# Performance work log

Hardware: AMD Instinct MI355X
Metric: run time of the kernel (lower is better)

Reference implementation:

```python
import jax, jax.numpy as jnp
import numpy as np

N = 50000      # nodes
E = 400000     # edges (avg degree 8)
N_IN = 256     # n_in_chan
N_HID = 256    # n_hid_chan


def gcn_conv(x, src, dst, W, b, n):
    """PyG GCNConv: D^{-1/2}(A+I)D^{-1/2} X W^T + b (add_self_loops=True, unit weights)."""
    h = x @ W.T                                           # [n, out]
    # degree over A + I: each node has a self loop (the initial ones) plus in-edges
    deg = jnp.ones((n,), h.dtype).at[dst].add(1.0)        # [n]
    dinv = jax.lax.rsqrt(deg)                             # deg >= 1 always
    norm = dinv[src] * dinv[dst]                          # [E]
    agg = jnp.zeros_like(h).at[dst].add(h[src] * norm[:, None])
    agg = agg + h * (dinv * dinv)[:, None]                # self-loop term, norm = dinv_i^2
    return agg + b


def setup_inputs() -> dict:
    key = jax.random.key(0)
    k1, k2, k3, k4 = jax.random.split(key, 4)
    x = jax.random.normal(k1, (N, N_IN + N_HID), dtype=jnp.float32)
    edge_index = jax.random.randint(k2, (2, E), 0, N, dtype=jnp.int64)
    s1 = 1.0 / np.sqrt(N_IN + N_HID)
    s2 = 1.0 / np.sqrt(N_HID)
    W1 = jax.random.normal(k3, (N_HID, N_IN + N_HID), dtype=jnp.float32) * s1
    W2 = jax.random.normal(k4, (N_HID, N_HID), dtype=jnp.float32) * s2
    b1 = jnp.zeros((N_HID,), jnp.float32)
    b2 = jnp.zeros((N_HID,), jnp.float32)
    return {"x": x, "edge_index": edge_index, "W1": W1, "b1": b1, "W2": W2, "b2": b2}


def reference(x, edge_index, W1, b1, W2, b2):
    src, dst = edge_index[0], edge_index[1]
    h = jax.nn.relu(gcn_conv(x, src, dst, W1, b1, N))
    return gcn_conv(h, src, dst, W2, b2, N)
```

## Files before the change

kernel.cpp:

```cpp
#include <hip/hip_runtime.h>
#include <hip/hip_bf16.h>

#define NN 50000
#define CH 256
#define SLOTS 96
#define G1K 512
#define G2K 256

typedef unsigned short u16;
typedef unsigned int   u32;

using short8 = __attribute__((ext_vector_type(8))) short;
using u16x8  = __attribute__((ext_vector_type(8))) unsigned short;
using f32x4  = __attribute__((ext_vector_type(4))) float;

static __device__ __forceinline__ float4 ld4(const float* p){ return *(const float4*)p; }

static __device__ __forceinline__ u16 f2b(float f){
  u32 u = __float_as_uint(f);
  u = (u + 0x7fffu + ((u >> 16) & 1u)) >> 16;
  return (u16)u;
}
static __device__ __forceinline__ float b2f(u16 b){
  return __uint_as_float(((u32)b) << 16);
}
static __device__ __forceinline__ int pkbf(float lo, float hi){
  __hip_bfloat162 h = __float22bfloat162_rn(make_float2(lo, hi));
  int r; __builtin_memcpy(&r, &h, 4); return r;
}

static __device__ __forceinline__ void gload_lds16(const void* g, void* l){
  __builtin_amdgcn_global_load_lds((const __attribute__((address_space(1))) void*)g,
                                   (__attribute__((address_space(3))) void*)l, 16, 0, 0);
}

#define WBAR(vm) do{ \
    asm volatile("s_waitcnt vmcnt(" #vm ") lgkmcnt(0)" ::: "memory"); \
    __builtin_amdgcn_s_barrier(); \
  }while(0)

#define SCHED0 __builtin_amdgcn_sched_barrier(0)


__global__ void ell_build_kernel(const int* __restrict__ src, const int* __restrict__ dst,
                                 int* __restrict__ deg, int* __restrict__ ell, int E,
                                 const float* __restrict__ W1, u16* __restrict__ W1bf, int w1n4,
                                 const float* __restrict__ W2, u16* __restrict__ W2bf, int w2n4){
  int T = gridDim.x * 256;
  int g = blockIdx.x*256 + threadIdx.x;
  if (g < E){
    int d = dst[g];
    int pos = atomicAdd(&deg[d], 1);
    if (pos < SLOTS) ell[(size_t)d*SLOTS + pos] = src[g];
  }
  for (int i = g; i < w1n4; i += T){
    float4 v = ld4(W1 + (size_t)i*4);
    int2 o = { pkbf(v.x,v.y), pkbf(v.z,v.w) };
    *(int2*)(W1bf + (size_t)i*4) = o;
  }
  for (int i = g; i < w2n4; i += T){
    float4 v = ld4(W2 + (size_t)i*4);
    int2 o = { pkbf(v.x,v.y), pkbf(v.z,v.w) };
    *(int2*)(W2bf + (size_t)i*4) = o;
  }
}


#define G1_GLB_B(kt, bb) do{ \
    gload_lds16(gB + (size_t)(kt)*32,          &Bs[bb][wave*2048]); \
    gload_lds16(gB + (size_t)(kt)*32 + 16*G1K, &Bs[bb][wave*2048 + 512]); \
    gload_lds16(gB + (size_t)(kt)*32 + 32*G1K, &Bs[bb][wave*2048 + 1024]); \
    gload_lds16(gB + (size_t)(kt)*32 + 48*G1K, &Bs[bb][wave*2048 + 1536]); \
    SCHED0; \
  }while(0)

#define G1_GLB_A(kt, ab) do{ \
    gload_lds16(gA0 + (size_t)(kt)*32, &Asf[ab][wave*512]); \
    gload_lds16(gA1 + (size_t)(kt)*32, &Asf[ab][wave*512 + 256]); \
    SCHED0; \
  }while(0)

#define G1_COMP(ra, rb) do{ \
    short8 af[4], bq[4]; \
    _Pragma("unroll") \
    for (int i=0;i<4;i++){ \
      int r = i*16 + lm; \
      float4 f0 = *(const float4*)&Asf[ra][r*32 + ((s0 ^ (lm&7))<<2)]; \
      float4 f1 = *(const float4*)&Asf[ra][r*32 + ((s1 ^ (lm&7))<<2)]; \
      int4 p = { pkbf(f0.x,f0.y), pkbf(f0.z,f0.w), pkbf(f1.x,f1.y), pkbf(f1.z,f1.w) }; \
      af[i] = *(short8*)&p; \
    } \
    _Pragma("unroll") \
    for (int j=0;j<4;j++) bq[j] = *(const short8*)&Bs[rb][(wave*64 + j*16 + lm)*32 + lk]; \
    _Pragma("unroll") \
    for (int i=0;i<4;i++) \
      _Pragma("unroll") \
      for (int j=0;j<4;j++) \
        acc[i][j] = __builtin_amdgcn_mfma_f32_16x16x32_bf16(af[i], bq[j], acc[i][j], 0, 0, 0); \
  }while(0)

__global__ __launch_bounds__(256, 2) void gemm1_kernel(const float* __restrict__ A,
                                                       const u16* __restrict__ Bbf,
                                                       const int* __restrict__ deg,
                                                       u16* __restrict__ C, int M){
  __shared__ float Asf[4][64*32];
  __shared__ u16   Bs[3][256*32];
  int tid = threadIdx.x;
  int wave = tid >> 6, lane = tid & 63;
  int bm = blockIdx.x;

  int cslot = (lane & 7) ^ (lane >> 3);
  int r0 = bm*64 + wave*16 + (lane>>3);     if (r0 > M-1) r0 = M-1;
  int r1 = r0 + 8;                          if (r1 > M-1) r1 = M-1;
  const float* gA0 = A + (size_t)r0*G1K + cslot*4;
  const float* gA1 = A + (size_t)r1*G1K + cslot*4;
  const u16* gB = Bbf + (size_t)(wave*64 + (lane>>2))*G1K + (lane&3)*8;

  int lm = lane & 15;
  int lk = (lane >> 4) * 8;
  int s0 = (lane >> 4) * 2;
  int s1 = s0 + 1;

  f32x4 acc[4][4] = {};

  G1_GLB_B(0, 0);
  G1_GLB_A(0, 0);
  G1_GLB_B(1, 1);
  G1_GLB_A(1, 1);
  G1_GLB_A(2, 2);
  WBAR(8);

  G1_GLB_B( 2,2); G1_COMP(0,0); G1_GLB_A( 3,3); WBAR(8);
  G1_GLB_B( 3,0); G1_COMP(1,1); G1_GLB_A( 4,0); WBAR(8);
  G1_GLB_B( 4,1); G1_COMP(2,2); G1_GLB_A( 5,1); WBAR(8);
  G1_GLB_B( 5,2); G1_COMP(3,0); G1_GLB_A( 6,2); WBAR(8);
  G1_GLB_B( 6,0); G1_COMP(0,1); G1_GLB_A( 7,3); WBAR(8);
  G1_GLB_B( 7,1); G1_COMP(1,2); G1_GLB_A( 8,0); WBAR(8);
  G1_GLB_B( 8,2); G1_COMP(2,0); G1_GLB_A( 9,1); WBAR(8);
  G1_GLB_B( 9,0); G1_COMP(3,1); G1_GLB_A(10,2); WBAR(8);
  G1_GLB_B(10,1); G1_COMP(0,2); G1_GLB_A(11,3); WBAR(8);
  G1_GLB_B(11,2); G1_COMP(1,0); G1_GLB_A(12,0); WBAR(8);
  G1_GLB_B(12,0); G1_COMP(2,1); G1_GLB_A(13,1); WBAR(8);
  G1_GLB_B(13,1); G1_COMP(3,2); G1_GLB_A(14,2); WBAR(8);
  G1_GLB_B(14,2); G1_COMP(0,0); G1_GLB_A(15,3); WBAR(8);
  G1_GLB_B(15,0); G1_COMP(1,1);                 WBAR(6);
                  G1_COMP(2,2);                 WBAR(0);
                  G1_COMP(3,0);

  int rb = (lane >> 4) * 4;
  #pragma unroll
  for (int i=0;i<4;i++){
    #pragma unroll
    for (int r=0;r<4;r++){
      int row = bm*64 + i*16 + rb + r;
      if (row < M){
        float dr = rsqrtf(1.0f + (float)deg[row]);
        #pragma unroll
        for (int j=0;j<4;j++){
          int col = wave*64 + j*16 + lm;
          C[(size_t)row*CH + col] = f2b(acc[i][j][r] * dr);
        }
      }
    }
  }
}


#define G2_GLB(kt, bb) do{ \
    gload_lds16(gA + (size_t)(kt)*32,          &As2[bb][wave*512]); \
    gload_lds16(gB + (size_t)(kt)*32,          &Bs2[bb][wave*2048]); \
    gload_lds16(gB + (size_t)(kt)*32 + 16*G2K, &Bs2[bb][wave*2048 + 512]); \
    gload_lds16(gB + (size_t)(kt)*32 + 32*G2K, &Bs2[bb][wave*2048 + 1024]); \
    gload_lds16(gB + (size_t)(kt)*32 + 48*G2K, &Bs2[bb][wave*2048 + 1536]); \
    SCHED0; \
  }while(0)

#define G2_COMP(rb) do{ \
    short8 af[4], bq[4]; \
    _Pragma("unroll") \
    for (int i=0;i<4;i++) af[i] = *(const short8*)&As2[rb][(i*16 + lm)*32 + lk]; \
    _Pragma("unroll") \
    for (int j=0;j<4;j++) bq[j] = *(const short8*)&Bs2[rb][(wave*64 + j*16 + lm)*32 + lk]; \
    _Pragma("unroll") \
    for (int i=0;i<4;i++) \
      _Pragma("unroll") \
      for (int j=0;j<4;j++) \
        acc[i][j] = __builtin_amdgcn_mfma_f32_16x16x32_bf16(af[i], bq[j], acc[i][j], 0, 0, 0); \
  }while(0)

__global__ __launch_bounds__(256, 4) void gemm2_kernel(const u16* __restrict__ A,
                                                       const u16* __restrict__ B,
                                                       float* __restrict__ Cout,
                                                       const float* __restrict__ bias, int M){
  __shared__ u16 As2[3][64*32];
  __shared__ u16 Bs2[3][256*32];
  int tid = threadIdx.x;
  int wave = tid >> 6, lane = tid & 63;
  int bm = blockIdx.x;

  int ar = bm*64 + wave*16 + (lane>>2); if (ar > M-1) ar = M-1;
  const u16* gA = A + (size_t)ar*G2K + (lane&3)*8;
  const u16* gB = B + (size_t)(wave*64 + (lane>>2))*G2K + (lane&3)*8;

  int lm = lane & 15;
  int lk = (lane >> 4) * 8;

  f32x4 acc[4][4] = {};

  G2_GLB(0, 0);
  G2_GLB(1, 1);
  WBAR(5);

  G2_GLB(2,2); G2_COMP(0); WBAR(5);
  G2_GLB(3,0); G2_COMP(1); WBAR(5);
  G2_GLB(4,1); G2_COMP(2); WBAR(5);
  G2_GLB(5,2); G2_COMP(0); WBAR(5);
  G2_GLB(6,0); G2_COMP(1); WBAR(5);
  G2_GLB(7,1); G2_COMP(2); WBAR(5);
               G2_COMP(0); WBAR(0);
               G2_COMP(1);

  float bv[4];
  #pragma unroll
  for (int j=0;j<4;j++) bv[j] = bias[wave*64 + j*16 + lm];

  int rb = (lane >> 4) * 4;
  #pragma unroll
  for (int i=0;i<4;i++){
    #pragma unroll
    for (int r=0;r<4;r++){
      int row = bm*64 + i*16 + rb + r;
      if (row < M){
        #pragma unroll
        for (int j=0;j<4;j++){
          int col = wave*64 + j*16 + lm;
          Cout[(size_t)row*CH + col] = acc[i][j][r] + bv[j];
        }
      }
    }
  }
}


template<bool RELU, bool BIAS, bool SCALEOUT>
__global__ __launch_bounds__(256) void aggregate_kernel(const u16* __restrict__ h,
                                                        const float* __restrict__ bias,
                                                        const int* __restrict__ deg,
                                                        const int* __restrict__ ell,
                                                        u16* __restrict__ outv, int n){
  int wave = threadIdx.x >> 6;
  int lane = threadIdx.x & 63;
  int i = blockIdx.x*4 + wave;
  if (i >= n) return;
  i = __builtin_amdgcn_readfirstlane(i);

  int degi = deg[i];
  float di = rsqrtf(1.0f + (float)degi);
  int m = degi < SLOTS ? degi : SLOTS;
  const int* __restrict__ row = ell + (size_t)i*SLOTS;
  int c = lane * 4;

  float a0=0.f, a1=0.f, a2=0.f, a3=0.f;

  int e = 0;
  for (; e + 3 < m; e += 4){
    int j0 = row[e], j1 = row[e+1], j2 = row[e+2], j3 = row[e+3];
    ushort4 h0 = *(const ushort4*)(h + (size_t)j0*CH + c);
    ushort4 h1 = *(const ushort4*)(h + (size_t)j1*CH + c);
    ushort4 h2 = *(const ushort4*)(h + (size_t)j2*CH + c);
    ushort4 h3 = *(const ushort4*)(h + (size_t)j3*CH + c);
    a0 += b2f(h0.x) + b2f(h1.x) + b2f(h2.x) + b2f(h3.x);
    a1 += b2f(h0.y) + b2f(h1.y) + b2f(h2.y) + b2f(h3.y);
    a2 += b2f(h0.z) + b2f(h1.z) + b2f(h2.z) + b2f(h3.z);
    a3 += b2f(h0.w) + b2f(h1.w) + b2f(h2.w) + b2f(h3.w);
  }
  for (; e < m; ++e){
    int j0 = row[e];
    ushort4 h0 = *(const ushort4*)(h + (size_t)j0*CH + c);
    a0 += b2f(h0.x); a1 += b2f(h0.y); a2 += b2f(h0.z); a3 += b2f(h0.w);
  }

  ushort4 hv = *(const ushort4*)(h + (size_t)i*CH + c);
  a0 += b2f(hv.x); a1 += b2f(hv.y); a2 += b2f(hv.z); a3 += b2f(hv.w);

  float v0 = a0*di, v1 = a1*di, v2 = a2*di, v3 = a3*di;
  if (BIAS){
    float4 b = ld4(bias + c);
    v0 += b.x; v1 += b.y; v2 += b.z; v3 += b.w;
  }
  if (RELU){
    v0 = fmaxf(v0, 0.f); v1 = fmaxf(v1, 0.f);
    v2 = fmaxf(v2, 0.f); v3 = fmaxf(v3, 0.f);
  }
  if (SCALEOUT){ v0 *= di; v1 *= di; v2 *= di; v3 *= di; }

  ushort4 o; o.x = f2b(v0); o.y = f2b(v1); o.z = f2b(v2); o.w = f2b(v3);
  *(ushort4*)(outv + (size_t)i*CH + c) = o;
}


extern "C" void kernel_launch(void* const* d_in, const int* in_sizes, int n_in,
                              void* d_out, int out_size, void* d_ws, size_t ws_size,
                              hipStream_t stream){
  const float* x  = (const float*)d_in[0];
  const int*   ei = (const int*)d_in[1];
  const float* W1 = (const float*)d_in[2];
  const float* b1 = (const float*)d_in[3];
  const float* W2 = (const float*)d_in[4];
  const float* b2 = (const float*)d_in[5];
  float* out = (float*)d_out;

  const int n = NN;
  const int E = in_sizes[1] / 2;
  const int* src = ei;
  const int* dst = ei + E;

  char* ws = (char*)d_ws;
  size_t off = 0;
  auto alloc = [&](size_t bytes)->char* {
    char* p = ws + off;
    off += (bytes + 255) & ~(size_t)255;
    return p;
  };
  u16*   h1bf   = (u16*)  alloc((size_t)n*CH*sizeof(u16));
  u16*   h2bf   = (u16*)  alloc((size_t)n*CH*sizeof(u16));
  u16*   W1bf   = (u16*)  alloc((size_t)CH*G1K*sizeof(u16));
  u16*   W2bf   = (u16*)  alloc((size_t)CH*CH*sizeof(u16));
  int*   deg    = (int*)  alloc((size_t)n*sizeof(int));
  int*   ell    = (int*)  alloc((size_t)n*SLOTS*sizeof(int));
  (void)ws_size;

  u16* g1out = (u16*)d_out;

  hipMemsetAsync(deg, 0, (size_t)n*sizeof(int), stream);
  ell_build_kernel<<<(E+255)/256, 256, 0, stream>>>(src, dst, deg, ell, E,
                                                    W1, W1bf, CH*G1K/4,
                                                    W2, W2bf, CH*CH/4);

  dim3 gg((n+63)/64);

  gemm1_kernel<<<gg, 256, 0, stream>>>(x, W1bf, deg, g1out, n);
  aggregate_kernel<true, true, true><<<(n+3)/4, 256, 0, stream>>>(g1out, b1, deg, ell, h1bf, n);

  aggregate_kernel<false, false, false><<<(n+3)/4, 256, 0, stream>>>(h1bf, b2, deg, ell, h2bf, n);
  gemm2_kernel<<<gg, 256, 0, stream>>>(h2bf, W2bf, out, b2, n);
}
```

Measured before the change: 306.7 us.

## Preload whole A tile into LDS as bf16 and use 8-wave 2x4 GEMM grid

Both GEMM kernels now run 512 threads (8 waves split 2x4 over M and N) instead of 4 waves. Each block first loads its entire 64-row A tile into LDS with an XOR swizzle, and only the B tiles are streamed through a triple buffer. In gemm1 the fp32-to-bf16 conversion of A now happens once at load time rather than being repeated by every wave on each k-step. The cost is that the A preload is no longer overlapped with MFMA work. gemm1 also needs about 112KB of LDS per block, which likely caps occupancy at one block per CU.

Result: slower. 322.4 us (+5.1%).

```diff
diff --git a/kernel.cpp b/kernel.cpp
--- a/kernel.cpp
+++ b/kernel.cpp
@@ -66,98 +66,100 @@
 }
 
 
-#define G1_GLB_B(kt, bb) do{ \
-    gload_lds16(gB + (size_t)(kt)*32,          &Bs[bb][wave*2048]); \
-    gload_lds16(gB + (size_t)(kt)*32 + 16*G1K, &Bs[bb][wave*2048 + 512]); \
-    gload_lds16(gB + (size_t)(kt)*32 + 32*G1K, &Bs[bb][wave*2048 + 1024]); \
-    gload_lds16(gB + (size_t)(kt)*32 + 48*G1K, &Bs[bb][wave*2048 + 1536]); \
+#define G1_GLB(kt, bb) do{ \
+    gload_lds16(gB + (size_t)(kt)*32,          &Bs[bb][wave*1024]); \
+    gload_lds16(gB + (size_t)(kt)*32 + 16*G1K, &Bs[bb][wave*1024 + 512]); \
     SCHED0; \
   }while(0)
 
-#define G1_GLB_A(kt, ab) do{ \
-    gload_lds16(gA0 + (size_t)(kt)*32, &Asf[ab][wave*512]); \
-    gload_lds16(gA1 + (size_t)(kt)*32, &Asf[ab][wave*512 + 256]); \
-    SCHED0; \
-  }while(0)
-
-#define G1_COMP(ra, rb) do{ \
-    short8 af[4], bq[4]; \
-    _Pragma("unroll") \
-    for (int i=0;i<4;i++){ \
-      int r = i*16 + lm; \
-      float4 f0 = *(const float4*)&Asf[ra][r*32 + ((s0 ^ (lm&7))<<2)]; \
-      float4 f1 = *(const float4*)&Asf[ra][r*32 + ((s1 ^ (lm&7))<<2)]; \
-      int4 p = { pkbf(f0.x,f0.y), pkbf(f0.z,f0.w), pkbf(f1.x,f1.y), pkbf(f1.z,f1.w) }; \
-      af[i] = *(short8*)&p; \
+#define G1_COMP(tt, rb) do{ \
+    short8 af[2], bq[4]; \
+    _Pragma("unroll") \
+    for (int i=0;i<2;i++){ \
+      int rr = wm*32 + i*16 + lm; \
+      af[i] = *(const short8*)&As[rr*512 + ((((tt)*8 + hi2) ^ xlm)<<2)]; \
     } \
     _Pragma("unroll") \
-    for (int j=0;j<4;j++) bq[j] = *(const short8*)&Bs[rb][(wave*64 + j*16 + lm)*32 + lk]; \
-    _Pragma("unroll") \
-    for (int i=0;i<4;i++) \
+    for (int j=0;j<4;j++) bq[j] = *(const short8*)&Bs[rb][(wn*64 + j*16 + lm)*32 + lk]; \
+    _Pragma("unroll") \
+    for (int i=0;i<2;i++) \
       _Pragma("unroll") \
       for (int j=0;j<4;j++) \
         acc[i][j] = __builtin_amdgcn_mfma_f32_16x16x32_bf16(af[i], bq[j], acc[i][j], 0, 0, 0); \
   }while(0)
 
-__global__ __launch_bounds__(256, 2) void gemm1_kernel(const float* __restrict__ A,
+__global__ __launch_bounds__(512, 2) void gemm1_kernel(const float* __restrict__ A,
                                                        const u16* __restrict__ Bbf,
                                                        const int* __restrict__ deg,
                                                        u16* __restrict__ C, int M){
-  __shared__ float Asf[4][64*32];
-  __shared__ u16   Bs[3][256*32];
+  __shared__ u16 As[64*512];
+  __shared__ u16 Bs[3][256*32];
   int tid = threadIdx.x;
   int wave = tid >> 6, lane = tid & 63;
   int bm = blockIdx.x;
 
-  int cslot = (lane & 7) ^ (lane >> 3);
-  int r0 = bm*64 + wave*16 + (lane>>3);     if (r0 > M-1) r0 = M-1;
-  int r1 = r0 + 8;                          if (r1 > M-1) r1 = M-1;
-  const float* gA0 = A + (size_t)r0*G1K + cslot*4;
-  const float* gA1 = A + (size_t)r1*G1K + cslot*4;
-  const u16* gB = Bbf + (size_t)(wave*64 + (lane>>2))*G1K + (lane&3)*8;
-
-  int lm = lane & 15;
-  int lk = (lane >> 4) * 8;
-  int s0 = (lane >> 4) * 2;
-  int s1 = s0 + 1;
-
-  f32x4 acc[4][4] = {};
-
-  G1_GLB_B(0, 0);
-  G1_GLB_A(0, 0);
-  G1_GLB_B(1, 1);
-  G1_GLB_A(1, 1);
-  G1_GLB_A(2, 2);
-  WBAR(8);
-
-  G1_GLB_B( 2,2); G1_COMP(0,0); G1_GLB_A( 3,3); WBAR(8);
-  G1_GLB_B( 3,0); G1_COMP(1,1); G1_GLB_A( 4,0); WBAR(8);
-  G1_GLB_B( 4,1); G1_COMP(2,2); G1_GLB_A( 5,1); WBAR(8);
-  G1_GLB_B( 5,2); G1_COMP(3,0); G1_GLB_A( 6,2); WBAR(8);
-  G1_GLB_B( 6,0); G1_COMP(0,1); G1_GLB_A( 7,3); WBAR(8);
-  G1_GLB_B( 7,1); G1_COMP(1,2); G1_GLB_A( 8,0); WBAR(8);
-  G1_GLB_B( 8,2); G1_COMP(2,0); G1_GLB_A( 9,1); WBAR(8);
-  G1_GLB_B( 9,0); G1_COMP(3,1); G1_GLB_A(10,2); WBAR(8);
-  G1_GLB_B(10,1); G1_COMP(0,2); G1_GLB_A(11,3); WBAR(8);
-  G1_GLB_B(11,2); G1_COMP(1,0); G1_GLB_A(12,0); WBAR(8);
-  G1_GLB_B(12,0); G1_COMP(2,1); G1_GLB_A(13,1); WBAR(8);
-  G1_GLB_B(13,1); G1_COMP(3,2); G1_GLB_A(14,2); WBAR(8);
-  G1_GLB_B(14,2); G1_COMP(0,0); G1_GLB_A(15,3); WBAR(8);
-  G1_GLB_B(15,0); G1_COMP(1,1);                 WBAR(6);
-                  G1_COMP(2,2);                 WBAR(0);
-                  G1_COMP(3,0);
-
-  int rb = (lane >> 4) * 4;
+  int wm = wave & 1, wn = wave >> 1;
+  int lm  = lane & 15;
+  int lk  = (lane >> 4) * 8;
+  int hi2 = (lane >> 4) * 2;
+  int xlm = (lm & 7) << 1;
+
   #pragma unroll
-  for (int i=0;i<4;i++){
+  for (int p=0; p<2; ++p){
+    float4 av[8];
+    #pragma unroll
+    for (int u=0; u<8; ++u){
+      int g = tid + (p*8+u)*512;
+      int lrow = g >> 7;
+      int grow = bm*64 + lrow; if (grow > M-1) grow = M-1;
+      av[u] = ld4(A + (size_t)grow*G1K + (g & 127)*4);
+    }
+    #pragma unroll
+    for (int u=0; u<8; ++u){
+      int g = tid + (p*8+u)*512;
+      int lrow = g >> 7;
+      int col4 = g & 127;
+      int2 o = { pkbf(av[u].x, av[u].y), pkbf(av[u].z, av[u].w) };
+      *(int2*)&As[lrow*512 + ((col4 ^ ((lrow & 7) << 1)) << 2)] = o;
+    }
+  }
+
+  const u16* gB = Bbf + (size_t)(wave*32 + (lane>>2))*G1K + (lane&3)*8;
+
+  f32x4 acc[2][4] = {};
+
+  G1_GLB(0, 0);
+  G1_GLB(1, 1);
+  WBAR(2);
+
+  G1_GLB( 2,2); G1_COMP( 0,0); WBAR(2);
+  G1_GLB( 3,0); G1_COMP( 1,1); WBAR(2);
+  G1_GLB( 4,1); G1_COMP( 2,2); WBAR(2);
+  G1_GLB( 5,2); G1_COMP( 3,0); WBAR(2);
+  G1_GLB( 6,0); G1_COMP( 4,1); WBAR(2);
+  G1_GLB( 7,1); G1_COMP( 5,2); WBAR(2);
+  G1_GLB( 8,2); G1_COMP( 6,0); WBAR(2);
+  G1_GLB( 9,0); G1_COMP( 7,1); WBAR(2);
+  G1_GLB(10,1); G1_COMP( 8,2); WBAR(2);
+  G1_GLB(11,2); G1_COMP( 9,0); WBAR(2);
+  G1_GLB(12,0); G1_COMP(10,1); WBAR(2);
+  G1_GLB(13,1); G1_COMP(11,2); WBAR(2);
+  G1_GLB(14,2); G1_COMP(12,0); WBAR(2);
+  G1_GLB(15,0); G1_COMP(13,1); WBAR(2);
+                G1_COMP(14,2); WBAR(0);
+                G1_COMP(15,0);
+
+  int rb4 = (lane >> 4) * 4;
+  #pragma unroll
+  for (int i=0;i<2;i++){
     #pragma unroll
     for (int r=0;r<4;r++){
-      int row = bm*64 + i*16 + rb + r;
+      int row = bm*64 + wm*32 + i*16 + rb4 + r;
       if (row < M){
         float dr = rsqrtf(1.0f + (float)deg[row]);
         #pragma unroll
         for (int j=0;j<4;j++){
-          int col = wave*64 + j*16 + lm;
+          int col = wn*64 + j*16 + lm;
           C[(size_t)row*CH + col] = f2b(acc[i][j][r] * dr);
         }
       }
@@ -167,73 +169,92 @@
 
 
 #define G2_GLB(kt, bb) do{ \
-    gload_lds16(gA + (size_t)(kt)*32,          &As2[bb][wave*512]); \
-    gload_lds16(gB + (size_t)(kt)*32,          &Bs2[bb][wave*2048]); \
-    gload_lds16(gB + (size_t)(kt)*32 + 16*G2K, &Bs2[bb][wave*2048 + 512]); \
-    gload_lds16(gB + (size_t)(kt)*32 + 32*G2K, &Bs2[bb][wave*2048 + 1024]); \
-    gload_lds16(gB + (size_t)(kt)*32 + 48*G2K, &Bs2[bb][wave*2048 + 1536]); \
+    gload_lds16(gB + (size_t)(kt)*32,          &Bs2[bb][wave*1024]); \
+    gload_lds16(gB + (size_t)(kt)*32 + 16*G2K, &Bs2[bb][wave*1024 + 512]); \
     SCHED0; \
   }while(0)
 
-#define G2_COMP(rb) do{ \
-    short8 af[4], bq[4]; \
-    _Pragma("unroll") \
-    for (int i=0;i<4;i++) af[i] = *(const short8*)&As2[rb][(i*16 + lm)*32 + lk]; \
-    _Pragma("unroll") \
-    for (int j=0;j<4;j++) bq[j] = *(const short8*)&Bs2[rb][(wave*64 + j*16 + lm)*32 + lk]; \
-    _Pragma("unroll") \
-    for (int i=0;i<4;i++) \
+#define G2_COMP(tt, rb) do{ \
+    short8 af[2], bq[4]; \
+    _Pragma("unroll") \
+    for (int i=0;i<2;i++){ \
+      int rr = wm*32 + i*16 + lm; \
+      af[i] = *(const short8*)&As2[rr*256 + ((((tt)*8 + hi2) ^ xlm)<<2)]; \
+    } \
+    _Pragma("unroll") \
+    for (int j=0;j<4;j++) bq[j] = *(const short8*)&Bs2[rb][(wn*64 + j*16 + lm)*32 + lk]; \
+    _Pragma("unroll") \
+    for (int i=0;i<2;i++) \
       _Pragma("unroll") \
       for (int j=0;j<4;j++) \
         acc[i][j] = __builtin_amdgcn_mfma_f32_16x16x32_bf16(af[i], bq[j], acc[i][j], 0, 0, 0); \
   }while(0)
 
-__global__ __launch_bounds__(256, 4) void gemm2_kernel(const u16* __restrict__ A,
+__global__ __launch_bounds__(512, 2) void gemm2_kernel(const u16* __restrict__ A,
                                                        const u16* __restrict__ B,
                                                        float* __restrict__ Cout,
                                                        const float* __restrict__ bias, int M){
-  __shared__ u16 As2[3][64*32];
+  __shared__ u16 As2[64*256];
   __shared__ u16 Bs2[3][256*32];
   int tid = threadIdx.x;
   int wave = tid >> 6, lane = tid & 63;
   int bm = blockIdx.x;
 
-  int ar = bm*64 + wave*16 + (lane>>2); if (ar > M-1) ar = M-1;
-  const u16* gA = A + (size_t)ar*G2K + (lane&3)*8;
-  const u16* gB = B + (size_t)(wave*64 + (lane>>2))*G2K + (lane&3)*8;
-
-  int lm = lane & 15;
-  int lk = (lane >> 4) * 8;
-
-  f32x4 acc[4][4] = {};
+  int wm = wave & 1, wn = wave >> 1;
+  int lm  = lane & 15;
+  int lk  = (lane >> 4) * 8;
+  int hi2 = (lane >> 4) * 2;
+  int xlm = (lm & 7) << 1;
+
+  {
+    u16x8 av[4];
+    #pragma unroll
+    for (int u=0; u<4; ++u){
+      int id = tid + u*512;
+      int lrow = id >> 5;
+      int grow = bm*64 + lrow; if (grow > M-1) grow = M-1;
+      av[u] = *(const u16x8*)(A + (size_t)grow*G2K + (id & 31)*8);
+    }
+    #pragma unroll
+    for (int u=0; u<4; ++u){
+      int id = tid + u*512;
+      int lrow = id >> 5;
+      int slot4 = (id & 31) * 2;
+      *(u16x8*)&As2[lrow*256 + ((slot4 ^ ((lrow & 7) << 1)) << 2)] = av[u];
+    }
+  }
+
+  const u16* gB = B + (size_t)(wave*32 + (lane>>2))*G2K + (lane&3)*8;
+
+  f32x4 acc[2][4] = {};
 
   G2_GLB(0, 0);
   G2_GLB(1, 1);
-  WBAR(5);
-
-  G2_GLB(2,2); G2_COMP(0); WBAR(5);
-  G2_GLB(3,0); G2_COMP(1); WBAR(5);
-  G2_GLB(4,1); G2_COMP(2); WBAR(5);
-  G2_GLB(5,2); G2_COMP(0); WBAR(5);
-  G2_GLB(6,0); G2_COMP(1); WBAR(5);
-  G2_GLB(7,1); G2_COMP(2); WBAR(5);
-               G2_COMP(0); WBAR(0);
-               G2_COMP(1);
+  WBAR(2);
+
+  G2_GLB(2,2); G2_COMP(0,0); WBAR(2);
+  G2_GLB(3,0); G2_COMP(1,1); WBAR(2);
+  G2_GLB(4,1); G2_COMP(2,2); WBAR(2);
+  G2_GLB(5,2); G2_COMP(3,0); WBAR(2);
+  G2_GLB(6,0); G2_COMP(4,1); WBAR(2);
+  G2_GLB(7,1); G2_COMP(5,2); WBAR(2);
+               G2_COMP(6,0); WBAR(0);
+               G2_COMP(7,1);
 
   float bv[4];
   #pragma unroll
-  for (int j=0;j<4;j++) bv[j] = bias[wave*64 + j*16 + lm];
-
-  int rb = (lane >> 4) * 4;
+  for (int j=0;j<4;j++) bv[j] = bias[wn*64 + j*16 + lm];
+
+  int rb4 = (lane >> 4) * 4;
   #pragma unroll
-  for (int i=0;i<4;i++){
+  for (int i=0;i<2;i++){
     #pragma unroll
     for (int r=0;r<4;r++){
-      int row = bm*64 + i*16 + rb + r;
+      int row = bm*64 + wm*32 + i*16 + rb4 + r;
       if (row < M){
         #pragma unroll
         for (int j=0;j<4;j++){
-          int col = wave*64 + j*16 + lm;
+          int col = wn*64 + j*16 + lm;
           Cout[(size_t)row*CH + col] = acc[i][j][r] + bv[j];
         }
       }
@@ -339,9 +360,9 @@
 
   dim3 gg((n+63)/64);
 
-  gemm1_kernel<<<gg, 256, 0, stream>>>(x, W1bf, deg, g1out, n);
+  gemm1_kernel<<<gg, 512, 0, stream>>>(x, W1bf, deg, g1out, n);
   aggregate_kernel<true, true, true><<<(n+3)/4, 256, 0, stream>>>(g1out, b1, deg, ell, h1bf, n);
 
   aggregate_kernel<false, false, false><<<(n+3)/4, 256, 0, stream>>>(h1bf, b2, deg, ell, h2bf, n);
-  gemm2_kernel<<<gg, 256, 0, stream>>>(h2bf, W2bf, out, b2, n);
-}
+  gemm2_kernel<<<gg, 512, 0, stream>>>(h2bf, W2bf, out, b2, n);
+}
```
